# Kernel optimization log

Hardware: AMD Instinct MI355X
Metric: run time of the kernel (lower is better)

Reference implementation:

```python
import jax, jax.numpy as jnp
import numpy as np

E, H, F, K = 8, 1024, 4096, 2  # experts, hidden, intermediate, top-k
B, S = 4, 2048


def setup_inputs() -> dict:
    key = jax.random.key(0)
    ks = jax.random.split(key, 6)
    x = jax.random.normal(ks[0], (B, S, H), dtype=jnp.float32)
    gate_w = jax.random.normal(ks[1], (H, E), dtype=jnp.float32) * 0.02
    gate_b = jnp.zeros((E,), dtype=jnp.float32)
    Wg = jax.random.normal(ks[2], (E, H, F), dtype=jnp.float32) * 0.02
    Wu = jax.random.normal(ks[3], (E, H, F), dtype=jnp.float32) * 0.02
    Wd = jax.random.normal(ks[4], (E, F, H), dtype=jnp.float32) * 0.02
    return {"x": x, "gate_w": gate_w, "gate_b": gate_b, "Wg": Wg, "Wu": Wu, "Wd": Wd}


def _moe_forward(x, gate_w, gate_b, Wg, Wu, Wd):
    xf = x.reshape(-1, x.shape[-1])                      # [T, H]
    T = xf.shape[0]
    logits = xf @ gate_w + gate_b                        # [T, E]  (gate_logit)
    top_vals, top_idx = jax.lax.top_k(logits, K)         # [T, K]
    # scatter top-k logits into -inf background, softmax -> zero weight for unselected experts
    sparse = jnp.full_like(logits, -jnp.inf)
    sparse = sparse.at[jnp.arange(T)[:, None], top_idx].set(top_vals)
    gate_weights = jax.nn.softmax(sparse, axis=-1)       # [T, E], exactly 0 off top-k

    # sum_e w_e * Expert_e(x); scan over the small expert axis to bound memory
    def expert_step(acc, params):
        wg, wu, wd, w = params                           # wg:[H,F] wu:[H,F] wd:[F,H] w:[T]
        h = jax.nn.silu(xf @ wg) * (xf @ wu)             # [T, F]
        y = h @ wd                                       # [T, H]
        return acc + w[:, None] * y, None

    acc0 = jnp.zeros_like(xf)
    acc, _ = jax.lax.scan(expert_step, acc0, (Wg, Wu, Wd, gate_weights.T))
    return acc.reshape(x.shape), logits


def reference(x, gate_w, gate_b, Wg, Wu, Wd):
    return _moe_forward(x, gate_w, gate_b, Wg, Wu, Wd)
```

## Files before the change

kernel.cpp:

```cpp
#include <hip/hip_runtime.h>
#include <cstdint>

#define TTOK 8192
#define HID  1024
#define FFD  4096
#define NEXP 8
#define NASSIGN 16384
#define MAXMB 24

typedef __attribute__((ext_vector_type(8))) short bf16x8;
typedef __attribute__((ext_vector_type(4))) float f32x4;

__device__ __forceinline__ unsigned short f2bf(float f) {
  unsigned int u = __builtin_bit_cast(unsigned int, f);
  u += 0x7FFFu + ((u >> 16) & 1u);
  return (unsigned short)(u >> 16);
}

__device__ __forceinline__ float bf2f(unsigned short s) {
  unsigned int u = (unsigned int)s << 16;
  return __builtin_bit_cast(float, u);
}

__device__ __forceinline__ void gload16(const unsigned short* g, unsigned short* l) {
  __builtin_amdgcn_global_load_lds(
      (const __attribute__((address_space(1))) unsigned int*)g,
      (__attribute__((address_space(3))) unsigned int*)l, 16, 0, 0);
}


__global__ void zero_counts_kernel(int* counts) {
  if (threadIdx.x < NEXP) counts[threadIdx.x] = 0;
}

__global__ void gate_kernel(const float* __restrict__ x,
                            const float* __restrict__ gw,
                            const float* __restrict__ gb,
                            float* __restrict__ logits_out,
                            int* __restrict__ counts,
                            int* __restrict__ te, int* __restrict__ tp,
                            float* __restrict__ tw,
                            unsigned short* __restrict__ xb) {
  const int lane = threadIdx.x & 63;
  const int wib  = threadIdx.x >> 6;
  const int t = blockIdx.x * 4 + wib;
  const float* xr = x + (size_t)t * HID;
  unsigned short* xbr = xb + (size_t)t * HID;

  float acc[NEXP];
#pragma unroll
  for (int e = 0; e < NEXP; ++e) acc[e] = 0.f;

#pragma unroll
  for (int i = 0; i < HID / 64; ++i) {
    int h = lane + 64 * i;
    float xv = xr[h];
    xbr[h] = f2bf(xv);
    const float* g = gw + h * NEXP;
#pragma unroll
    for (int e = 0; e < NEXP; ++e) acc[e] += xv * g[e];
  }
#pragma unroll
  for (int off = 32; off; off >>= 1)
#pragma unroll
    for (int e = 0; e < NEXP; ++e) acc[e] += __shfl_xor(acc[e], off);
#pragma unroll
  for (int e = 0; e < NEXP; ++e) acc[e] += gb[e];

  if (lane < NEXP) logits_out[(size_t)t * NEXP + lane] = acc[lane];

  if (lane == 0) {
    int e0 = 0; float v0 = acc[0];
#pragma unroll
    for (int e = 1; e < NEXP; ++e) if (acc[e] > v0) { v0 = acc[e]; e0 = e; }
    int e1 = -1; float v1 = -3.4e38f;
#pragma unroll
    for (int e = 0; e < NEXP; ++e) if (e != e0 && acc[e] > v1) { v1 = acc[e]; e1 = e; }
    float s = __expf(v1 - v0);
    float w0 = 1.f / (1.f + s);
    float w1 = s * w0;
    int p0 = atomicAdd(&counts[e0], 1);
    int p1 = atomicAdd(&counts[e1], 1);
    te[t * 2] = e0; te[t * 2 + 1] = e1;
    tp[t * 2] = p0; tp[t * 2 + 1] = p1;
    tw[t * 2] = w0; tw[t * 2 + 1] = w1;
  }
}

__global__ void scatter_kernel(const int* __restrict__ counts, int* __restrict__ offsets,
                               const int* __restrict__ te, const int* __restrict__ tp,
                               const float* __restrict__ tw,
                               int* __restrict__ tok_of, float* __restrict__ wt_of,
                               int* __restrict__ asn_of) {
  __shared__ int offs[NEXP];
  if (threadIdx.x == 0) {
    int run = 0;
    for (int e = 0; e < NEXP; ++e) { offs[e] = run; offsets[e] = run; run += counts[e]; }
  }
  __syncthreads();
  for (int t = threadIdx.x; t < TTOK; t += blockDim.x) {
#pragma unroll
    for (int j = 0; j < 2; ++j) {
      int e = te[t * 2 + j];
      int a = offs[e] + tp[t * 2 + j];
      tok_of[a] = t;
      wt_of[a] = tw[t * 2 + j];
      asn_of[t * 2 + j] = a;
    }
  }
}


__global__ void transpose_all_kernel(const float* __restrict__ Wg,
                                     const float* __restrict__ Wu,
                                     const float* __restrict__ Wd,
                                     unsigned short* __restrict__ WgT,
                                     unsigned short* __restrict__ WuT,
                                     unsigned short* __restrict__ WdT) {
  const int which = blockIdx.y;
  const int e = blockIdx.z;
  const float* src;
  unsigned short* dst;
  int R, C, tr, tc;
  if (which == 0)      { src = Wg; dst = WgT; R = HID; C = FFD; }
  else if (which == 1) { src = Wu; dst = WuT; R = HID; C = FFD; }
  else                 { src = Wd; dst = WdT; R = FFD; C = HID; }
  if (which < 2) { tc = blockIdx.x & 63; tr = blockIdx.x >> 6; }
  else           { tc = blockIdx.x & 15; tr = blockIdx.x >> 4; }
  const size_t base = (size_t)e * (size_t)R * C;
  src += base; dst += base;
  const int r0 = tr * 64, c0 = tc * 64;

  __shared__ float tile[64][65];
  const int tid = threadIdx.x;
  {
    const int c4 = (tid & 15) * 4, rr = tid >> 4;
#pragma unroll
    for (int i = 0; i < 4; ++i) {
      int row = rr + i * 16;
      float4 v = *(const float4*)&src[(size_t)(r0 + row) * C + c0 + c4];
      tile[row][c4 + 0] = v.x; tile[row][c4 + 1] = v.y;
      tile[row][c4 + 2] = v.z; tile[row][c4 + 3] = v.w;
    }
  }
  __syncthreads();
  {
    const int r4 = (tid & 15) * 4, cc = tid >> 4;
#pragma unroll
    for (int i = 0; i < 4; ++i) {
      int c = cc + i * 16;
      ushort4 o;
      o.x = f2bf(tile[r4 + 0][c]);
      o.y = f2bf(tile[r4 + 1][c]);
      o.z = f2bf(tile[r4 + 2][c]);
      o.w = f2bf(tile[r4 + 3][c]);
      *(ushort4*)&dst[(size_t)(c0 + c) * R + r0 + r4] = o;
    }
  }
}


__global__ __launch_bounds__(256, 2) void moe_up_kernel(
    const unsigned short* __restrict__ xb,
    const unsigned short* __restrict__ WgT,
    const unsigned short* __restrict__ WuT,
    const int* __restrict__ counts, const int* __restrict__ offsets,
    const int* __restrict__ tok_of,
    unsigned short* __restrict__ hbuf)
{
  const int e = blockIdx.x & 7;
  const int mblk = blockIdx.x >> 3;
  const int cnt = counts[e];
  if (mblk * 128 >= cnt) return;
  const int off = offsets[e];
  const int n0 = blockIdx.y * 128;

  __shared__ __align__(16) unsigned short As[2][128 * 32];
  __shared__ __align__(16) unsigned short Bgs[2][128 * 32];
  __shared__ __align__(16) unsigned short Bus[2][128 * 32];
  __shared__ int toks[128];

  const int tid = threadIdx.x;
  const int lane = tid & 63;
  const int w = tid >> 6;

  if (tid < 128) {
    int a = off + mblk * 128 + tid;
    if (a > NASSIGN - 1) a = NASSIGN - 1;
    toks[tid] = tok_of[a];
  }
  __syncthreads();

  const unsigned short* asrc[2];
  const unsigned short* bgsrc[2];
  const unsigned short* busrc[2];
#pragma unroll
  for (int j = 0; j < 2; ++j) {
    int rrow = w * 32 + j * 16 + (lane >> 2);
    int kcol = 8 * (lane & 3);
    asrc[j]  = xb  + (size_t)toks[rrow] * HID + kcol;
    bgsrc[j] = WgT + ((size_t)e * FFD + n0 + rrow) * HID + kcol;
    busrc[j] = WuT + ((size_t)e * FFD + n0 + rrow) * HID + kcol;
  }

  auto STAGE = [&](int buf, int k0) {
#pragma unroll
    for (int j = 0; j < 2; ++j) {
      gload16(asrc[j]  + k0, &As[buf][w * 1024 + j * 512]);
      gload16(bgsrc[j] + k0, &Bgs[buf][w * 1024 + j * 512]);
      gload16(busrc[j] + k0, &Bus[buf][w * 1024 + j * 512]);
    }
  };

  f32x4 accg[4][4] = {};
  f32x4 accu[4][4] = {};
  const int wr = (w >> 1) * 64, wc = (w & 1) * 64;
  const int lr = lane & 15, kg = (lane >> 4) * 8;

  STAGE(0, 0);
#pragma unroll 1
  for (int t = 0; t < HID / 32; ++t) {
    const int cur = t & 1;
    if (t + 1 < HID / 32) {
      STAGE(cur ^ 1, (t + 1) * 32);
      asm volatile("s_waitcnt vmcnt(6)" ::: "memory");
    } else {
      asm volatile("s_waitcnt vmcnt(0)" ::: "memory");
    }
    __builtin_amdgcn_s_barrier();

    bf16x8 af[4], bgf[4], buf_[4];
#pragma unroll
    for (int m = 0; m < 4; ++m)
      af[m] = *(const bf16x8*)&As[cur][(wr + m * 16 + lr) * 32 + kg];
#pragma unroll
    for (int n = 0; n < 4; ++n) {
      bgf[n]  = *(const bf16x8*)&Bgs[cur][(wc + n * 16 + lr) * 32 + kg];
      buf_[n] = *(const bf16x8*)&Bus[cur][(wc + n * 16 + lr) * 32 + kg];
    }
#pragma unroll
    for (int m = 0; m < 4; ++m)
#pragma unroll
      for (int n = 0; n < 4; ++n) {
        accg[m][n] = __builtin_amdgcn_mfma_f32_16x16x32_bf16(af[m], bgf[n],  accg[m][n], 0, 0, 0);
        accu[m][n] = __builtin_amdgcn_mfma_f32_16x16x32_bf16(af[m], buf_[n], accu[m][n], 0, 0, 0);
      }
    __builtin_amdgcn_s_barrier();
  }

  const int crb = (lane >> 4) * 4, cc = lane & 15;
#pragma unroll
  for (int m = 0; m < 4; ++m)
#pragma unroll
    for (int n = 0; n < 4; ++n)
#pragma unroll
      for (int r = 0; r < 4; ++r) {
        int lrow = wr + m * 16 + crb + r;
        int grow = mblk * 128 + lrow;
        if (grow < cnt) {
          size_t a = (size_t)off + grow;
          float g = accg[m][n][r];
          float u = accu[m][n][r];
          float sg = g / (1.0f + __expf(-g));
          hbuf[a * FFD + (n0 + wc + n * 16 + cc)] = f2bf(sg * u);
        }
      }
}

__global__ __launch_bounds__(256, 2) void moe_down_kernel(
    const unsigned short* __restrict__ hb,
    const unsigned short* __restrict__ WdT,
    const int* __restrict__ counts, const int* __restrict__ offsets,
    unsigned short* __restrict__ ypart)
{
  const int e = blockIdx.x & 7;
  const int mblk = blockIdx.x >> 3;
  const int cnt = counts[e];
  if (mblk * 128 >= cnt) return;
  const int off = offsets[e];
  const int n0 = blockIdx.y * 128;

  __shared__ __align__(16) unsigned short As[2][128 * 32];
  __shared__ __align__(16) unsigned short Bs[2][128 * 32];

  const int tid = threadIdx.x;
  const int lane = tid & 63;
  const int w = tid >> 6;

  const unsigned short* asrc[2];
  const unsigned short* bsrc[2];
#pragma unroll
  for (int j = 0; j < 2; ++j) {
    int rrow = w * 32 + j * 16 + (lane >> 2);
    int kcol = 8 * (lane & 3);
    int a = off + mblk * 128 + rrow;
    if (a > NASSIGN - 1) a = NASSIGN - 1;
    asrc[j] = hb + (size_t)a * FFD + kcol;
    bsrc[j] = WdT + ((size_t)e * HID + n0 + rrow) * FFD + kcol;
  }

  auto STAGE = [&](int buf, int k0) {
#pragma unroll
    for (int j = 0; j < 2; ++j) {
      gload16(asrc[j] + k0, &As[buf][w * 1024 + j * 512]);
      gload16(bsrc[j] + k0, &Bs[buf][w * 1024 + j * 512]);
    }
  };

  f32x4 acc[4][4] = {};
  const int wr = (w >> 1) * 64, wc = (w & 1) * 64;
  const int lr = lane & 15, kg = (lane >> 4) * 8;

  STAGE(0, 0);
#pragma unroll 1
  for (int t = 0; t < FFD / 32; ++t) {
    const int cur = t & 1;
    if (t + 1 < FFD / 32) {
      STAGE(cur ^ 1, (t + 1) * 32);
      asm volatile("s_waitcnt vmcnt(4)" ::: "memory");
    } else {
      asm volatile("s_waitcnt vmcnt(0)" ::: "memory");
    }
    __builtin_amdgcn_s_barrier();

    bf16x8 af[4], bf_[4];
#pragma unroll
    for (int m = 0; m < 4; ++m)
      af[m] = *(const bf16x8*)&As[cur][(wr + m * 16 + lr) * 32 + kg];
#pragma unroll
    for (int n = 0; n < 4; ++n)
      bf_[n] = *(const bf16x8*)&Bs[cur][(wc + n * 16 + lr) * 32 + kg];
#pragma unroll
    for (int m = 0; m < 4; ++m)
#pragma unroll
      for (int n = 0; n < 4; ++n)
        acc[m][n] = __builtin_amdgcn_mfma_f32_16x16x32_bf16(af[m], bf_[n], acc[m][n], 0, 0, 0);
    __builtin_amdgcn_s_barrier();
  }

  const int crb = (lane >> 4) * 4, cc = lane & 15;
#pragma unroll
  for (int m = 0; m < 4; ++m)
#pragma unroll
    for (int n = 0; n < 4; ++n)
#pragma unroll
      for (int r = 0; r < 4; ++r) {
        int lrow = wr + m * 16 + crb + r;
        int grow = mblk * 128 + lrow;
        if (grow < cnt)
          ypart[((size_t)off + grow) * HID + (n0 + wc + n * 16 + cc)] = f2bf(acc[m][n][r]);
      }
}

__global__ void combine_kernel(const unsigned short* __restrict__ ypart,
                               const int* __restrict__ asn_of,
                               const float* __restrict__ wt_of,
                               float* __restrict__ y) {
  const int t = blockIdx.x;
  const int a0 = asn_of[t * 2], a1 = asn_of[t * 2 + 1];
  const float w0 = wt_of[a0], w1 = wt_of[a1];
  const int c = threadIdx.x * 4;
  ushort4 p0 = *(const ushort4*)&ypart[(size_t)a0 * HID + c];
  ushort4 p1 = *(const ushort4*)&ypart[(size_t)a1 * HID + c];
  float4 r;
  r.x = w0 * bf2f(p0.x) + w1 * bf2f(p1.x);
  r.y = w0 * bf2f(p0.y) + w1 * bf2f(p1.y);
  r.z = w0 * bf2f(p0.z) + w1 * bf2f(p1.z);
  r.w = w0 * bf2f(p0.w) + w1 * bf2f(p1.w);
  *(float4*)&y[(size_t)t * HID + c] = r;
}


extern "C" void kernel_launch(void* const* d_in, const int* in_sizes, int n_in,
                              void* d_out, int out_size, void* d_ws, size_t ws_size,
                              hipStream_t stream) {
  const float* x  = (const float*)d_in[0];
  const float* gw = (const float*)d_in[1];
  const float* gb = (const float*)d_in[2];
  const float* Wg = (const float*)d_in[3];
  const float* Wu = (const float*)d_in[4];
  const float* Wd = (const float*)d_in[5];
  float* out = (float*)d_out;
  float* logits = out + (size_t)TTOK * HID;

  char* ws = (char*)d_ws;
  size_t o = 0;
  auto carve = [&](size_t b) { char* p = ws + o; o += (b + 255) & ~(size_t)255; return p; };
  int*   counts  = (int*)carve(NEXP * 4);
  int*   offsets = (int*)carve(NEXP * 4);
  int*   te      = (int*)carve((size_t)TTOK * 2 * 4);
  int*   tp      = (int*)carve((size_t)TTOK * 2 * 4);
  float* tw      = (float*)carve((size_t)TTOK * 2 * 4);
  int*   tok_of  = (int*)carve((size_t)NASSIGN * 4);
  float* wt_of   = (float*)carve((size_t)NASSIGN * 4);
  int*   asn_of  = (int*)carve((size_t)TTOK * 2 * 4);
  unsigned short* xb  = (unsigned short*)carve((size_t)TTOK * HID * 2);
  unsigned short* WgT = (unsigned short*)carve((size_t)NEXP * FFD * HID * 2);
  unsigned short* WuT = (unsigned short*)carve((size_t)NEXP * FFD * HID * 2);
  unsigned short* WdT = (unsigned short*)carve((size_t)NEXP * HID * FFD * 2);
  unsigned short* hb  = (unsigned short*)carve((size_t)NASSIGN * FFD * 2);
  unsigned short* ypart = (unsigned short*)carve((size_t)NASSIGN * HID * 2);
  (void)ws_size; (void)in_sizes; (void)n_in; (void)out_size;

  zero_counts_kernel<<<dim3(1), dim3(64), 0, stream>>>(counts);
  gate_kernel<<<dim3(TTOK / 4), dim3(256), 0, stream>>>(x, gw, gb, logits, counts, te, tp, tw, xb);
  scatter_kernel<<<dim3(1), dim3(256), 0, stream>>>(counts, offsets, te, tp, tw, tok_of, wt_of, asn_of);
  transpose_all_kernel<<<dim3(1024, 3, NEXP), dim3(256), 0, stream>>>(Wg, Wu, Wd, WgT, WuT, WdT);
  moe_up_kernel<<<dim3(NEXP * MAXMB, FFD / 128), dim3(256), 0, stream>>>(xb, WgT, WuT, counts, offsets, tok_of, hb);
  moe_down_kernel<<<dim3(NEXP * MAXMB, HID / 128), dim3(256), 0, stream>>>(hb, WdT, counts, offsets, ypart);
  combine_kernel<<<dim3(TTOK), dim3(256), 0, stream>>>(ypart, asn_of, wt_of, out);
}
```

Before: 965.3 us.

## Rewrite down-projection GEMM with 256x256 tiles, 4-stage pipeline and swizzled LDS

The down-projection kernel moves from 128x128 tiles with 256 threads and double buffering to 256x256 tiles with 512 threads and a 4-deep LDS ring. Global-to-LDS loads are issued three stages ahead and split into A and B halves that interleave with two MFMA phases per K step. It also adds an XOR swizzle on LDS columns to avoid bank conflicts, plus s_setprio around the MFMA bursts. The larger tile cuts redundant reloads of hb and WdT, but it launches fewer blocks (MCAP=12 caps the blocks per expert) and uses 128 KB of LDS per block, which lowers occupancy and may underfill the GPU.

```diff
diff --git a/kernel.cpp b/kernel.cpp
--- a/kernel.cpp
+++ b/kernel.cpp
@@ -7,6 +7,7 @@
 #define NEXP 8
 #define NASSIGN 16384
 #define MAXMB 24
+#define MCAP 12
 
 typedef __attribute__((ext_vector_type(8))) short bf16x8;
 typedef __attribute__((ext_vector_type(4))) float f32x4;
@@ -267,7 +268,8 @@
       }
 }
 
-__global__ __launch_bounds__(256, 2) void moe_down_kernel(
+
+__global__ __launch_bounds__(512, 1) void moe_down_kernel(
     const unsigned short* __restrict__ hb,
     const unsigned short* __restrict__ WdT,
     const int* __restrict__ counts, const int* __restrict__ offsets,
@@ -276,79 +278,99 @@
   const int e = blockIdx.x & 7;
   const int mblk = blockIdx.x >> 3;
   const int cnt = counts[e];
-  if (mblk * 128 >= cnt) return;
+  if (mblk * 256 >= cnt) return;
   const int off = offsets[e];
-  const int n0 = blockIdx.y * 128;
-
-  __shared__ __align__(16) unsigned short As[2][128 * 32];
-  __shared__ __align__(16) unsigned short Bs[2][128 * 32];
+  const int n0 = blockIdx.y * 256;
+
+  __shared__ __align__(16) unsigned short L[4][16384];
 
   const int tid = threadIdx.x;
   const int lane = tid & 63;
   const int w = tid >> 6;
 
-  const unsigned short* asrc[2];
-  const unsigned short* bsrc[2];
-#pragma unroll
-  for (int j = 0; j < 2; ++j) {
-    int rrow = w * 32 + j * 16 + (lane >> 2);
-    int kcol = 8 * (lane & 3);
-    int a = off + mblk * 128 + rrow;
-    if (a > NASSIGN - 1) a = NASSIGN - 1;
-    asrc[j] = hb + (size_t)a * FFD + kcol;
-    bsrc[j] = WdT + ((size_t)e * HID + n0 + rrow) * FFD + kcol;
-  }
-
-  auto STAGE = [&](int buf, int k0) {
-#pragma unroll
-    for (int j = 0; j < 2; ++j) {
-      gload16(asrc[j] + k0, &As[buf][w * 1024 + j * 512]);
-      gload16(bsrc[j] + k0, &Bs[buf][w * 1024 + j * 512]);
-    }
+  const int sr = tid >> 2, st = tid & 3;
+  const int scol = ((st ^ ((sr >> 1) & 3)) << 3);
+  int ar0 = off + mblk * 256 + sr;       if (ar0 > NASSIGN - 1) ar0 = NASSIGN - 1;
+  int ar1 = off + mblk * 256 + 128 + sr; if (ar1 > NASSIGN - 1) ar1 = NASSIGN - 1;
+  const unsigned short* a0p = hb + (size_t)ar0 * FFD + scol;
+  const unsigned short* a1p = hb + (size_t)ar1 * FFD + scol;
+  const unsigned short* b0p = WdT + ((size_t)e * HID + n0 + sr) * FFD + scol;
+  const unsigned short* b1p = WdT + ((size_t)e * HID + n0 + 128 + sr) * FFD + scol;
+
+  auto SP0 = [&](int g) {
+    unsigned short* H = &L[g & 3][0];
+    gload16(a0p + g * 32, H + tid * 8);
+    gload16(a1p + g * 32, H + 4096 + tid * 8);
   };
-
-  f32x4 acc[4][4] = {};
-  const int wr = (w >> 1) * 64, wc = (w & 1) * 64;
-  const int lr = lane & 15, kg = (lane >> 4) * 8;
-
-  STAGE(0, 0);
-#pragma unroll 1
-  for (int t = 0; t < FFD / 32; ++t) {
-    const int cur = t & 1;
-    if (t + 1 < FFD / 32) {
-      STAGE(cur ^ 1, (t + 1) * 32);
-      asm volatile("s_waitcnt vmcnt(4)" ::: "memory");
-    } else {
-      asm volatile("s_waitcnt vmcnt(0)" ::: "memory");
-    }
+  auto SP1 = [&](int g) {
+    unsigned short* H = &L[g & 3][0];
+    gload16(b0p + g * 32, H + 8192 + tid * 8);
+    gload16(b1p + g * 32, H + 12288 + tid * 8);
+  };
+
+  const int lr = lane & 15, lq = lane >> 4;
+  const int rdswz = ((lq ^ ((lr >> 1) & 3)) << 3);
+  const int wm = w >> 2, wn = w & 3;
+
+  f32x4 acc[8][4] = {};
+
+  SP0(0); SP1(0); SP0(1); SP1(1); SP0(2); SP1(2);
+
+  const int NH = FFD / 32;
+  bf16x8 bf_[4];
+#pragma unroll 4
+  for (int g = 0; g < NH; ++g) {
+    const unsigned short* H = &L[g & 3][0];
+    const int rem = NH - 1 - g;
+    if (rem >= 2)      asm volatile("s_waitcnt vmcnt(8)" ::: "memory");
+    else if (rem == 1) asm volatile("s_waitcnt vmcnt(4)" ::: "memory");
+    else               asm volatile("s_waitcnt vmcnt(0)" ::: "memory");
     __builtin_amdgcn_s_barrier();
 
-    bf16x8 af[4], bf_[4];
-#pragma unroll
-    for (int m = 0; m < 4; ++m)
-      af[m] = *(const bf16x8*)&As[cur][(wr + m * 16 + lr) * 32 + kg];
+    bf16x8 af[4];
+#pragma unroll
+    for (int m = 0; m < 4; ++m)
+      af[m] = *(const bf16x8*)(H + (wm * 128 + m * 16 + lr) * 32 + rdswz);
 #pragma unroll
     for (int n = 0; n < 4; ++n)
-      bf_[n] = *(const bf16x8*)&Bs[cur][(wc + n * 16 + lr) * 32 + kg];
+      bf_[n] = *(const bf16x8*)(H + 8192 + (wn * 64 + n * 16 + lr) * 32 + rdswz);
+    if (g + 3 < NH) SP0(g + 3);
+    asm volatile("s_waitcnt lgkmcnt(0)" ::: "memory");
+    __builtin_amdgcn_s_setprio(1);
 #pragma unroll
     for (int m = 0; m < 4; ++m)
 #pragma unroll
       for (int n = 0; n < 4; ++n)
         acc[m][n] = __builtin_amdgcn_mfma_f32_16x16x32_bf16(af[m], bf_[n], acc[m][n], 0, 0, 0);
+    __builtin_amdgcn_s_setprio(0);
     __builtin_amdgcn_s_barrier();
+
+#pragma unroll
+    for (int m = 0; m < 4; ++m)
+      af[m] = *(const bf16x8*)(H + (wm * 128 + 64 + m * 16 + lr) * 32 + rdswz);
+    if (g + 3 < NH) SP1(g + 3);
+    __builtin_amdgcn_s_barrier();
+    asm volatile("s_waitcnt lgkmcnt(0)" ::: "memory");
+    __builtin_amdgcn_s_setprio(1);
+#pragma unroll
+    for (int m = 0; m < 4; ++m)
+#pragma unroll
+      for (int n = 0; n < 4; ++n)
+        acc[4 + m][n] = __builtin_amdgcn_mfma_f32_16x16x32_bf16(af[m], bf_[n], acc[4 + m][n], 0, 0, 0);
+    __builtin_amdgcn_s_setprio(0);
   }
 
   const int crb = (lane >> 4) * 4, cc = lane & 15;
 #pragma unroll
-  for (int m = 0; m < 4; ++m)
+  for (int m = 0; m < 8; ++m)
 #pragma unroll
     for (int n = 0; n < 4; ++n)
 #pragma unroll
       for (int r = 0; r < 4; ++r) {
-        int lrow = wr + m * 16 + crb + r;
-        int grow = mblk * 128 + lrow;
+        int lrow = wm * 128 + (m >> 2) * 64 + (m & 3) * 16 + crb + r;
+        int grow = mblk * 256 + lrow;
         if (grow < cnt)
-          ypart[((size_t)off + grow) * HID + (n0 + wc + n * 16 + cc)] = f2bf(acc[m][n][r]);
+          ypart[((size_t)off + grow) * HID + (n0 + wn * 64 + n * 16 + cc)] = f2bf(acc[m][n][r]);
       }
 }
 
@@ -407,6 +429,6 @@
   scatter_kernel<<<dim3(1), dim3(256), 0, stream>>>(counts, offsets, te, tp, tw, tok_of, wt_of, asn_of);
   transpose_all_kernel<<<dim3(1024, 3, NEXP), dim3(256), 0, stream>>>(Wg, Wu, Wd, WgT, WuT, WdT);
   moe_up_kernel<<<dim3(NEXP * MAXMB, FFD / 128), dim3(256), 0, stream>>>(xb, WgT, WuT, counts, offsets, tok_of, hb);
-  moe_down_kernel<<<dim3(NEXP * MAXMB, HID / 128), dim3(256), 0, stream>>>(hb, WdT, counts, offsets, ypart);
+  moe_down_kernel<<<dim3(NEXP * MCAP, HID / 256), dim3(512), 0, stream>>>(hb, WdT, counts, offsets, ypart);
   combine_kernel<<<dim3(TTOK), dim3(256), 0, stream>>>(ypart, asn_of, wt_of, out);
 }
```

New measurement: 946.1 us (median of 2 runs). -2.0%, faster.

## Widen down-projection tile to 128x256 and vectorize gate and transpose stores

Applied to the files above, without the earlier changes.

The down-projection GEMM tile grows from 128x128 to 128x256 output columns, so each block reuses its A (hidden activation) tile across twice as many columns and half as many blocks reload hb. Each wave now holds 4x8 accumulators, which raises register and LDS pressure and halves the grid. The gate kernel now reads x as float4 and writes bf16 in ushort4 chunks. The transpose kernel writes 16-byte bf16 chunks instead of 8-byte ones.

```diff
diff --git a/kernel.cpp b/kernel.cpp
--- a/kernel.cpp
+++ b/kernel.cpp
@@ -52,13 +52,17 @@
   for (int e = 0; e < NEXP; ++e) acc[e] = 0.f;
 
 #pragma unroll
-  for (int i = 0; i < HID / 64; ++i) {
-    int h = lane + 64 * i;
-    float xv = xr[h];
-    xbr[h] = f2bf(xv);
-    const float* g = gw + h * NEXP;
-#pragma unroll
-    for (int e = 0; e < NEXP; ++e) acc[e] += xv * g[e];
+  for (int i = 0; i < HID / 256; ++i) {
+    const int h = lane * 4 + i * 256;
+    float4 xv = *(const float4*)(xr + h);
+    ushort4 o;
+    o.x = f2bf(xv.x); o.y = f2bf(xv.y); o.z = f2bf(xv.z); o.w = f2bf(xv.w);
+    *(ushort4*)(xbr + h) = o;
+    const float* g0 = gw + (size_t)h * NEXP;
+#pragma unroll
+    for (int e = 0; e < NEXP; ++e)
+      acc[e] += xv.x * g0[e] + xv.y * g0[NEXP + e]
+              + xv.z * g0[2 * NEXP + e] + xv.w * g0[3 * NEXP + e];
   }
 #pragma unroll
   for (int off = 32; off; off >>= 1)
@@ -145,16 +149,14 @@
   }
   __syncthreads();
   {
-    const int r4 = (tid & 15) * 4, cc = tid >> 4;
-#pragma unroll
-    for (int i = 0; i < 4; ++i) {
-      int c = cc + i * 16;
-      ushort4 o;
-      o.x = f2bf(tile[r4 + 0][c]);
-      o.y = f2bf(tile[r4 + 1][c]);
-      o.z = f2bf(tile[r4 + 2][c]);
-      o.w = f2bf(tile[r4 + 3][c]);
-      *(ushort4*)&dst[(size_t)(c0 + c) * R + r0 + r4] = o;
+    const int r8 = (tid & 7) * 8, chi = tid >> 3;
+#pragma unroll
+    for (int i = 0; i < 2; ++i) {
+      int c = chi + i * 32;
+      union { unsigned short us[8]; uint4 v; } o;
+#pragma unroll
+      for (int j = 0; j < 8; ++j) o.us[j] = f2bf(tile[r8 + j][c]);
+      *(uint4*)&dst[(size_t)(c0 + c) * R + r0 + r8] = o.v;
     }
   }
 }
@@ -267,6 +269,7 @@
       }
 }
 
+
 __global__ __launch_bounds__(256, 2) void moe_down_kernel(
     const unsigned short* __restrict__ hb,
     const unsigned short* __restrict__ WdT,
@@ -278,17 +281,17 @@
   const int cnt = counts[e];
   if (mblk * 128 >= cnt) return;
   const int off = offsets[e];
-  const int n0 = blockIdx.y * 128;
+  const int n0 = blockIdx.y * 256;
 
   __shared__ __align__(16) unsigned short As[2][128 * 32];
-  __shared__ __align__(16) unsigned short Bs[2][128 * 32];
+  __shared__ __align__(16) unsigned short Bs[2][256 * 32];
 
   const int tid = threadIdx.x;
   const int lane = tid & 63;
   const int w = tid >> 6;
 
   const unsigned short* asrc[2];
-  const unsigned short* bsrc[2];
+  const unsigned short* bsrc[4];
 #pragma unroll
   for (int j = 0; j < 2; ++j) {
     int rrow = w * 32 + j * 16 + (lane >> 2);
@@ -296,19 +299,25 @@
     int a = off + mblk * 128 + rrow;
     if (a > NASSIGN - 1) a = NASSIGN - 1;
     asrc[j] = hb + (size_t)a * FFD + kcol;
+  }
+#pragma unroll
+  for (int j = 0; j < 4; ++j) {
+    int rrow = w * 64 + j * 16 + (lane >> 2);
+    int kcol = 8 * (lane & 3);
     bsrc[j] = WdT + ((size_t)e * HID + n0 + rrow) * FFD + kcol;
   }
 
   auto STAGE = [&](int buf, int k0) {
 #pragma unroll
-    for (int j = 0; j < 2; ++j) {
+    for (int j = 0; j < 2; ++j)
       gload16(asrc[j] + k0, &As[buf][w * 1024 + j * 512]);
-      gload16(bsrc[j] + k0, &Bs[buf][w * 1024 + j * 512]);
-    }
+#pragma unroll
+    for (int j = 0; j < 4; ++j)
+      gload16(bsrc[j] + k0, &Bs[buf][w * 2048 + j * 512]);
   };
 
-  f32x4 acc[4][4] = {};
-  const int wr = (w >> 1) * 64, wc = (w & 1) * 64;
+  f32x4 acc[4][8] = {};
+  const int wr = (w >> 1) * 64, wc = (w & 1) * 128;
   const int lr = lane & 15, kg = (lane >> 4) * 8;
 
   STAGE(0, 0);
@@ -317,23 +326,23 @@
     const int cur = t & 1;
     if (t + 1 < FFD / 32) {
       STAGE(cur ^ 1, (t + 1) * 32);
-      asm volatile("s_waitcnt vmcnt(4)" ::: "memory");
+      asm volatile("s_waitcnt vmcnt(6)" ::: "memory");
     } else {
       asm volatile("s_waitcnt vmcnt(0)" ::: "memory");
     }
     __builtin_amdgcn_s_barrier();
 
-    bf16x8 af[4], bf_[4];
+    bf16x8 af[4], bf_[8];
 #pragma unroll
     for (int m = 0; m < 4; ++m)
       af[m] = *(const bf16x8*)&As[cur][(wr + m * 16 + lr) * 32 + kg];
 #pragma unroll
-    for (int n = 0; n < 4; ++n)
+    for (int n = 0; n < 8; ++n)
       bf_[n] = *(const bf16x8*)&Bs[cur][(wc + n * 16 + lr) * 32 + kg];
 #pragma unroll
     for (int m = 0; m < 4; ++m)
 #pragma unroll
-      for (int n = 0; n < 4; ++n)
+      for (int n = 0; n < 8; ++n)
         acc[m][n] = __builtin_amdgcn_mfma_f32_16x16x32_bf16(af[m], bf_[n], acc[m][n], 0, 0, 0);
     __builtin_amdgcn_s_barrier();
   }
@@ -342,7 +351,7 @@
 #pragma unroll
   for (int m = 0; m < 4; ++m)
 #pragma unroll
-    for (int n = 0; n < 4; ++n)
+    for (int n = 0; n < 8; ++n)
 #pragma unroll
       for (int r = 0; r < 4; ++r) {
         int lrow = wr + m * 16 + crb + r;
@@ -407,6 +416,6 @@
   scatter_kernel<<<dim3(1), dim3(256), 0, stream>>>(counts, offsets, te, tp, tw, tok_of, wt_of, asn_of);
   transpose_all_kernel<<<dim3(1024, 3, NEXP), dim3(256), 0, stream>>>(Wg, Wu, Wd, WgT, WuT, WdT);
   moe_up_kernel<<<dim3(NEXP * MAXMB, FFD / 128), dim3(256), 0, stream>>>(xb, WgT, WuT, counts, offsets, tok_of, hb);
-  moe_down_kernel<<<dim3(NEXP * MAXMB, HID / 128), dim3(256), 0, stream>>>(hb, WdT, counts, offsets, ypart);
+  moe_down_kernel<<<dim3(NEXP * MAXMB, HID / 256), dim3(256), 0, stream>>>(hb, WdT, counts, offsets, ypart);
   combine_kernel<<<dim3(TTOK), dim3(256), 0, stream>>>(ypart, asn_of, wt_of, out);
 }
```

Measured after the change: 1.006 ms. 4.2% more time.
